# Performance work log

Measured on AMD Instinct MI355X. Metric: run time of the kernel, lower is better.

Reference implementation:

```python
import jax, jax.numpy as jnp
import numpy as np

B, S, D, H, E, K = 4, 2048, 768, 3072, 8, 2
LB_SCALE = 0.01
NOISY_STD = 1.0


def setup_inputs() -> dict:
    key = jax.random.key(0)
    ks = jax.random.split(key, 8)
    x = jax.random.normal(ks[0], (B, S, D), jnp.float32)
    # gate_linear: nn.Linear(D, E, bias=False); torch weight is [E, D]
    gate_w = jax.random.normal(ks[1], (E, D), jnp.float32) * 0.02
    noise_weight = jnp.zeros((E,), jnp.float32)  # initialized to zeros in torch
    noise = jax.random.normal(ks[2], (B, S, E), jnp.float32)  # torch.randn_like(logits)
    # expert weights stored in (in, out) layout: y = x @ w + b
    w1 = jax.random.normal(ks[3], (E, D, H), jnp.float32) * 0.02
    b1 = jnp.zeros((E, H), jnp.float32)
    w2 = jax.random.normal(ks[4], (E, D, H), jnp.float32) * 0.02
    b2 = jnp.zeros((E, H), jnp.float32)
    wp = jax.random.normal(ks[5], (E, H, D), jnp.float32) * 0.02
    bp = jnp.zeros((E, D), jnp.float32)
    return {"x": x, "gate_w": gate_w, "noise_weight": noise_weight, "noise": noise,
            "w1": w1, "b1": b1, "w2": w2, "b2": b2, "wp": wp, "bp": bp}


def reference(x, gate_w, noise_weight, noise, w1, b1, w2, b2, wp, bp):
    num_experts = gate_w.shape[0]
    # --- TopKGateParallel ---
    logits = jnp.einsum('bsd,ed->bse', x, gate_w)            # [B,S,E]
    gate_weights = jax.nn.softmax(logits, axis=-1)
    gate_weights_mean = gate_weights.reshape(-1, num_experts).mean(0)
    uniform = 1.0 / num_experts
    load_balance_loss = jnp.mean((gate_weights_mean - uniform) ** 2) * LB_SCALE
    logits_noisy = logits + noise * NOISY_STD * noise_weight  # noise_weight zeros => no-op at init
    top_k_vals, top_k_ids = jax.lax.top_k(logits_noisy, K)    # [B,S,K]
    # scatter top-k back into a -inf tensor, then softmax -> sparse gates
    topk_mask = jax.nn.one_hot(top_k_ids, num_experts, dtype=logits.dtype).sum(-2) > 0  # [B,S,E]
    sparse_logits = jnp.where(topk_mask, logits_noisy, -jnp.inf)
    gates = jax.nn.softmax(sparse_logits, axis=-1)            # zeros outside top-k
    # --- per-expert SwiGLU, weighted combine (gates are exactly 0 off top-k) ---
    y = jnp.zeros_like(x)
    for e in range(num_experts):  # small fixed expert count
        h = (x @ w1[e] + b1[e]) * jax.nn.silu(x @ w2[e] + b2[e])  # [B,S,H]
        y = y + gates[..., e:e + 1] * (h @ wp[e] + bp[e])
    return y, load_balance_loss
```

## Files before the change

kernel.cpp:

```cpp
#include <hip/hip_runtime.h>
#include <hip/hip_bf16.h>

#define NTOK 8192
#define DDIM 768
#define HDIM 3072
#define NEXP 8
#define MROWS (NTOK*2)
#define RBMAX 32

typedef float f32x4 __attribute__((ext_vector_type(4)));
typedef short bf16x8 __attribute__((ext_vector_type(8)));
typedef unsigned short u16x4 __attribute__((ext_vector_type(4)));

__device__ __forceinline__ unsigned short f2bf(float f) {
  union { float f; unsigned u; } v; v.f = f;
  unsigned r = v.u + 0x7fffu + ((v.u >> 16) & 1u);
  return (unsigned short)(r >> 16);
}

typedef __attribute__((address_space(3))) unsigned int* lds_ptr_t;
typedef const __attribute__((address_space(1))) unsigned int* gbl_ptr_t;
__device__ __forceinline__ void async16(const void* g, void* l) {
  __builtin_amdgcn_global_load_lds((gbl_ptr_t)g, (lds_ptr_t)l, 16, 0, 0);
}

__global__ __launch_bounds__(128) void gating_kernel(
    const float* __restrict__ x, const float* __restrict__ gw,
    const float* __restrict__ nw, const float* __restrict__ noise,
    int* counts, float* sums, int* tok_list, float* gate_list,
    int* tok_top, float* gate_top, int* pos_top)
{
  __shared__ float s_gw[NEXP*DDIM];
  __shared__ float s_sums[NEXP];
  __shared__ float s_nw[NEXP];
  int tid = threadIdx.x;
  for (int i = tid; i < NEXP*DDIM/4; i += 128)
    ((f32x4*)s_gw)[i] = ((const f32x4*)gw)[i];
  if (tid < NEXP) { s_sums[tid] = 0.f; s_nw[tid] = nw[tid]; }
  __syncthreads();
  int t = blockIdx.x*128 + tid;
  float acc[NEXP];
  #pragma unroll
  for (int e = 0; e < NEXP; ++e) acc[e] = 0.f;
  const f32x4* xr = (const f32x4*)(x + (size_t)t*DDIM);
  for (int d4 = 0; d4 < DDIM/4; ++d4) {
    f32x4 xv = xr[d4];
    #pragma unroll
    for (int e = 0; e < NEXP; ++e) {
      f32x4 g = *(const f32x4*)&s_gw[e*DDIM + d4*4];
      acc[e] += xv.x*g.x + xv.y*g.y + xv.z*g.z + xv.w*g.w;
    }
  }
  float m = acc[0];
  #pragma unroll
  for (int e = 1; e < NEXP; ++e) m = fmaxf(m, acc[e]);
  float p[NEXP], s = 0.f;
  #pragma unroll
  for (int e = 0; e < NEXP; ++e) { p[e] = __expf(acc[e]-m); s += p[e]; }
  float inv = 1.f/s;
  #pragma unroll
  for (int e = 0; e < NEXP; ++e) atomicAdd(&s_sums[e], p[e]*inv);
  float ln[NEXP];
  #pragma unroll
  for (int e = 0; e < NEXP; ++e) ln[e] = acc[e] + noise[(size_t)t*NEXP+e]*s_nw[e];
  int i0 = 0; float v0 = ln[0];
  #pragma unroll
  for (int e = 1; e < NEXP; ++e) if (ln[e] > v0) { v0 = ln[e]; i0 = e; }
  int i1 = -1; float v1 = 0.f;
  #pragma unroll
  for (int e = 0; e < NEXP; ++e)
    if (e != i0 && (i1 < 0 || ln[e] > v1)) { v1 = ln[e]; i1 = e; }
  float e1 = __expf(v1 - v0);
  float g0 = 1.f/(1.f + e1);
  float g1 = e1*g0;
  int p0 = atomicAdd(&counts[i0], 1);
  tok_list[i0*NTOK + p0] = t; gate_list[i0*NTOK + p0] = g0;
  int p1 = atomicAdd(&counts[i1], 1);
  tok_list[i1*NTOK + p1] = t; gate_list[i1*NTOK + p1] = g1;
  tok_top[2*t] = i0; tok_top[2*t+1] = i1;
  gate_top[2*t] = g0; gate_top[2*t+1] = g1;
  pos_top[2*t] = p0; pos_top[2*t+1] = p1;
  __syncthreads();
  if (tid < NEXP) atomicAdd(&sums[tid], s_sums[tid]);
}

__global__ void finalize_kernel(const int* counts, const float* sums,
                                int* offsets, float* loss_out)
{
  if (threadIdx.x == 0) {
    int o = 0;
    #pragma unroll
    for (int e = 0; e < NEXP; ++e) { offsets[e] = o; o += counts[e]; }
    offsets[NEXP] = o;
    float l = 0.f;
    #pragma unroll
    for (int e = 0; e < NEXP; ++e) {
      float dv = sums[e]*(1.f/(float)NTOK) - 1.f/(float)NEXP;
      l += dv*dv;
    }
    loss_out[0] = l*(0.01f/(float)NEXP);
  }
}

__global__ __launch_bounds__(256) void cvt_x_kernel(const float* __restrict__ x,
                                                    unsigned short* __restrict__ xb)
{
  int i = blockIdx.x*256 + threadIdx.x;
  f32x4 v = ((const f32x4*)x)[i];
  u16x4 o; o.x = f2bf(v.x); o.y = f2bf(v.y); o.z = f2bf(v.z); o.w = f2bf(v.w);
  ((u16x4*)xb)[i] = o;
}

__global__ __launch_bounds__(256) void transpose_cvt2_kernel(
    const float* __restrict__ src1, unsigned short* __restrict__ dst1,
    const float* __restrict__ src2, unsigned short* __restrict__ dst2,
    int R, int C)
{
  __shared__ unsigned short s[64*65];
  int z = blockIdx.z;
  int e = z & (NEXP-1);
  const float* src = (z < NEXP) ? src1 : src2;
  unsigned short* dst = (z < NEXP) ? dst1 : dst2;
  int r0 = blockIdx.y*64, c0 = blockIdx.x*64;
  const float* sp = src + ((size_t)e*R + r0)*C + c0;
  unsigned short* dp = dst + ((size_t)e*C + c0)*R + r0;
  int t = threadIdx.x;
  #pragma unroll
  for (int i = 0; i < 16; ++i) {
    int idx = t + 256*i;
    int r = idx >> 6, c = idx & 63;
    s[c*65 + r] = f2bf(sp[(size_t)r*C + c]);
  }
  __syncthreads();
  #pragma unroll
  for (int i = 0; i < 16; ++i) {
    int idx = t + 256*i;
    int c = idx >> 6, r = idx & 63;
    dp[(size_t)c*R + r] = s[c*65 + r];
  }
}

__global__ __launch_bounds__(256) void transpose_cvt_kernel(
    const float* __restrict__ src, unsigned short* __restrict__ dst, int R, int C)
{
  __shared__ unsigned short s[64*65];
  int e = blockIdx.z;
  int r0 = blockIdx.y*64, c0 = blockIdx.x*64;
  const float* sp = src + ((size_t)e*R + r0)*C + c0;
  unsigned short* dp = dst + ((size_t)e*C + c0)*R + r0;
  int t = threadIdx.x;
  #pragma unroll
  for (int i = 0; i < 16; ++i) {
    int idx = t + 256*i;
    int r = idx >> 6, c = idx & 63;
    s[c*65 + r] = f2bf(sp[(size_t)r*C + c]);
  }
  __syncthreads();
  #pragma unroll
  for (int i = 0; i < 16; ++i) {
    int idx = t + 256*i;
    int c = idx >> 6, r = idx & 63;
    dp[(size_t)c*R + r] = s[c*65 + r];
  }
}

__global__ __launch_bounds__(256) void compact_kernel(
    const int* __restrict__ counts, const int* __restrict__ offsets,
    const int* __restrict__ tok_list, const float* __restrict__ gate_list,
    int* __restrict__ row_token, float* __restrict__ row_gate)
{
  int e = blockIdx.y;
  int pos = blockIdx.x*256 + threadIdx.x;
  if (pos < counts[e]) {
    int r = offsets[e] + pos;
    row_token[r] = tok_list[e*NTOK + pos];
    row_gate[r]  = gate_list[e*NTOK + pos];
  }
}

__global__ __launch_bounds__(256) void init_y_kernel(
    const int* __restrict__ tok_top, const float* __restrict__ gate_top,
    const float* __restrict__ bp, float* __restrict__ y)
{
  int i = blockIdx.x*256 + threadIdx.x;
  int t = i / (DDIM/4);
  int d4 = i % (DDIM/4);
  int e0 = tok_top[2*t], e1 = tok_top[2*t+1];
  float g0 = gate_top[2*t], g1 = gate_top[2*t+1];
  f32x4 b0 = ((const f32x4*)(bp + (size_t)e0*DDIM))[d4];
  f32x4 b1v = ((const f32x4*)(bp + (size_t)e1*DDIM))[d4];
  ((f32x4*)y)[i] = g0*b0 + g1*b1v;
}

__global__ __launch_bounds__(256) void ffn1_mfma(
    const unsigned short* __restrict__ xb,
    const unsigned short* __restrict__ w1T, const unsigned short* __restrict__ w2T,
    const float* __restrict__ b1, const float* __restrict__ b2,
    const int* __restrict__ offsets, const int* __restrict__ row_token,
    unsigned short* __restrict__ h_buf, int h_base, int HC)
{
  int id = blockIdx.x;
  int e = id & 7;
  int s = id >> 3;
  int rb0 = s & (RBMAX-1);
  int cg = s >> 5;
  int r_lo = offsets[e];
  int rows_e = offsets[e+1] - r_lo;
  int h0 = h_base + cg*64;

  __shared__ __align__(16) char sA[8192];
  __shared__ __align__(16) char sB[8192];
  __shared__ int s_tok[128];

  int tid = threadIdx.x;
  int lane = tid & 63, w = tid >> 6;
  int l16 = lane & 15, quad = lane >> 4;
  int lr = lane >> 2, ls = lane & 3;
  int kseg = ls ^ (lr & 3);
  int fro = l16*64 + ((quad ^ (l16 & 3)) << 4);

  int colB = h0 + w*16 + lr;
  const unsigned short* gB1 = w1T + ((size_t)e*HDIM + colB)*DDIM + kseg*8;
  const unsigned short* gB2 = w2T + ((size_t)e*HDIM + colB)*DDIM + kseg*8;
  char* lA0 = sA + w*1024;
  char* lA1 = sA + (w+4)*1024;
  char* lB1 = sB + w*1024;
  char* lB2 = sB + (w+4)*1024;

  int hcol = h0 + w*16 + l16;
  float bb1 = b1[(size_t)e*HDIM + hcol];
  float bb2 = b2[(size_t)e*HDIM + hcol];
  int hl = hcol - h_base;

  for (int rb = rb0; rb*128 < rows_e; rb += RBMAX) {
    int r0 = r_lo + rb*128;
    int rows_valid = rows_e - rb*128; if (rows_valid > 128) rows_valid = 128;
    __syncthreads();
    if (tid < 128) {
      int r = r0 + tid; if (r > MROWS-1) r = MROWS-1;
      s_tok[tid] = row_token[r];
    }
    __syncthreads();
    const unsigned short* gA0 = xb + (size_t)s_tok[w*16 + lr]*DDIM + kseg*8;
    const unsigned short* gA1 = xb + (size_t)s_tok[(w+4)*16 + lr]*DDIM + kseg*8;

    f32x4 acc1[8], acc2[8];
    #pragma unroll
    for (int i = 0; i < 8; ++i) { acc1[i] = (f32x4){0,0,0,0}; acc2[i] = (f32x4){0,0,0,0}; }

    for (int k0 = 0; k0 < DDIM; k0 += 32) {
      async16(gA0 + k0, lA0);
      async16(gA1 + k0, lA1);
      async16(gB1 + k0, lB1);
      async16(gB2 + k0, lB2);
      __syncthreads();
      bf16x8 bf1 = *(const bf16x8*)(sB + w*1024 + fro);
      bf16x8 bf2 = *(const bf16x8*)(sB + (w+4)*1024 + fro);
      #pragma unroll
      for (int mt = 0; mt < 8; ++mt) {
        bf16x8 af = *(const bf16x8*)(sA + mt*1024 + fro);
        acc1[mt] = __builtin_amdgcn_mfma_f32_16x16x32_bf16(af, bf1, acc1[mt], 0, 0, 0);
        acc2[mt] = __builtin_amdgcn_mfma_f32_16x16x32_bf16(af, bf2, acc2[mt], 0, 0, 0);
      }
      __syncthreads();
    }
    #pragma unroll
    for (int mt = 0; mt < 8; ++mt) {
      #pragma unroll
      for (int r = 0; r < 4; ++r) {
        int row = mt*16 + quad*4 + r;
        if (row < rows_valid) {
          float c1 = acc1[mt][r] + bb1;
          float c2 = acc2[mt][r] + bb2;
          float hv = c1 * (c2 / (1.f + __expf(-c2)));
          h_buf[(size_t)(r0 + row)*HC + hl] = f2bf(hv);
        }
      }
    }
  }
}

__global__ __launch_bounds__(256) void ffn2_mfma(
    const unsigned short* __restrict__ h_buf, const unsigned short* __restrict__ wpT,
    const int* __restrict__ offsets, const int* __restrict__ row_token,
    const float* __restrict__ row_gate, float* __restrict__ outp,
    int h_base, int HC, int mode)
{
  int id = blockIdx.x;
  int e = id & 7;
  int s = id >> 3;
  int rb0 = s & (RBMAX-1);
  int cb = s >> 5;
  int r_lo = offsets[e];
  int rows_e = offsets[e+1] - r_lo;
  int c0 = cb*128;

  __shared__ __align__(16) char sA[8192];
  __shared__ __align__(16) char sB[8192];
  __shared__ int s_tok[128];
  __shared__ float s_gate[128];

  int tid = threadIdx.x;
  int lane = tid & 63, w = tid >> 6;
  int l16 = lane & 15, quad = lane >> 4;
  int lr = lane >> 2, ls = lane & 3;
  int kseg = ls ^ (lr & 3);
  int fro = l16*64 + ((quad ^ (l16 & 3)) << 4);
  int wr = w & 1, wcg = w >> 1;

  const unsigned short* gB0 = wpT + ((size_t)e*DDIM + c0 + w*16 + lr)*HDIM + h_base + kseg*8;
  const unsigned short* gB1 = wpT + ((size_t)e*DDIM + c0 + (w+4)*16 + lr)*HDIM + h_base + kseg*8;
  char* lA0 = sA + w*1024;
  char* lA1 = sA + (w+4)*1024;
  char* lB0 = sB + w*1024;
  char* lB1 = sB + (w+4)*1024;

  for (int rb = rb0; rb*128 < rows_e; rb += RBMAX) {
    int r0 = r_lo + rb*128;
    int rows_valid = rows_e - rb*128; if (rows_valid > 128) rows_valid = 128;
    __syncthreads();
    if (tid < 128) {
      int r = r0 + tid; if (r > MROWS-1) r = MROWS-1;
      s_tok[tid]  = row_token[r];
      s_gate[tid] = row_gate[r];
    }
    __syncthreads();
    int rA0 = r0 + w*16 + lr;     if (rA0 > MROWS-1) rA0 = MROWS-1;
    int rA1 = r0 + (w+4)*16 + lr; if (rA1 > MROWS-1) rA1 = MROWS-1;
    const unsigned short* gA0 = h_buf + (size_t)rA0*HC + kseg*8;
    const unsigned short* gA1 = h_buf + (size_t)rA1*HC + kseg*8;

    f32x4 acc[4][4];
    #pragma unroll
    for (int i = 0; i < 4; ++i)
      #pragma unroll
      for (int j = 0; j < 4; ++j) acc[i][j] = (f32x4){0,0,0,0};

    for (int k0 = 0; k0 < HC; k0 += 32) {
      async16(gA0 + k0, lA0);
      async16(gA1 + k0, lA1);
      async16(gB0 + k0, lB0);
      async16(gB1 + k0, lB1);
      __syncthreads();
      bf16x8 bfr[4];
      #pragma unroll
      for (int nt = 0; nt < 4; ++nt)
        bfr[nt] = *(const bf16x8*)(sB + (wcg*4 + nt)*1024 + fro);
      #pragma unroll
      for (int mt = 0; mt < 4; ++mt) {
        bf16x8 af = *(const bf16x8*)(sA + (wr*4 + mt)*1024 + fro);
        #pragma unroll
        for (int nt = 0; nt < 4; ++nt)
          acc[mt][nt] = __builtin_amdgcn_mfma_f32_16x16x32_bf16(af, bfr[nt], acc[mt][nt], 0, 0, 0);
      }
      __syncthreads();
    }

    if (mode == 0) {
      #pragma unroll
      for (int nt = 0; nt < 4; ++nt) {
        int col = c0 + wcg*64 + nt*16 + l16;
        #pragma unroll
        for (int mt = 0; mt < 4; ++mt) {
          #pragma unroll
          for (int r = 0; r < 4; ++r) {
            int row = wr*64 + mt*16 + quad*4 + r;
            if (row < rows_valid)
              outp[(size_t)(r0 + row)*DDIM + col] = acc[mt][nt][r];
          }
        }
      }
    } else {
      #pragma unroll
      for (int nt = 0; nt < 4; ++nt) {
        int col = c0 + wcg*64 + nt*16 + l16;
        #pragma unroll
        for (int mt = 0; mt < 4; ++mt) {
          #pragma unroll
          for (int r = 0; r < 4; ++r) {
            int row = wr*64 + mt*16 + quad*4 + r;
            if (row < rows_valid)
              atomicAdd(&outp[(size_t)s_tok[row]*DDIM + col], s_gate[row]*acc[mt][nt][r]);
          }
        }
      }
    }
  }
}

__global__ __launch_bounds__(256) void combine_kernel(
    const float* __restrict__ part, const int* __restrict__ tok_top,
    const float* __restrict__ gate_top, const int* __restrict__ pos_top,
    const int* __restrict__ offsets, const float* __restrict__ bp,
    float* __restrict__ y)
{
  int i = blockIdx.x*256 + threadIdx.x;
  int t = i / (DDIM/4);
  int d4 = i % (DDIM/4);
  int e0 = tok_top[2*t], e1 = tok_top[2*t+1];
  float g0 = gate_top[2*t], g1 = gate_top[2*t+1];
  int r0 = offsets[e0] + pos_top[2*t];
  int r1 = offsets[e1] + pos_top[2*t+1];
  f32x4 v0 = ((const f32x4*)part)[(size_t)r0*(DDIM/4) + d4];
  f32x4 v1 = ((const f32x4*)part)[(size_t)r1*(DDIM/4) + d4];
  f32x4 b0 = ((const f32x4*)(bp + (size_t)e0*DDIM))[d4];
  f32x4 b1v = ((const f32x4*)(bp + (size_t)e1*DDIM))[d4];
  ((f32x4*)y)[i] = g0*(v0 + b0) + g1*(v1 + b1v);
}

__global__ __launch_bounds__(256) void ffn2_kernel(
    const unsigned short* __restrict__ h_buf, const float* __restrict__ wp,
    const int* __restrict__ offsets, const int* __restrict__ row_token,
    const float* __restrict__ row_gate, float* __restrict__ y, int h_base, int HC)
{
  int e = blockIdx.z;
  int r_lo = offsets[e];
  int rows_e = offsets[e+1] - r_lo;
  int bx = blockIdx.x;
  if (bx*128 >= rows_e) return;
  int r0 = r_lo + bx*128;
  int rows_valid = rows_e - bx*128; if (rows_valid > 128) rows_valid = 128;
  int c0 = blockIdx.y*128;

  __shared__ unsigned short sA[128*40];
  __shared__ int s_tok[128];
  __shared__ float s_gate[128];

  int tid = threadIdx.x;
  if (tid < 128) {
    int r = r0 + tid; if (r > MROWS-1) r = MROWS-1;
    s_tok[tid]  = row_token[r];
    s_gate[tid] = row_gate[r];
  }
  int lane = tid & 63;
  int wc = tid >> 6;
  int quad = lane >> 4, l16 = lane & 15;

  const float* wp0 = wp + (size_t)e*HDIM*DDIM + c0 + wc*32 + l16;

  f32x4 acc[8][2];
  #pragma unroll
  for (int i = 0; i < 8; ++i) { acc[i][0] = (f32x4){0,0,0,0}; acc[i][1] = (f32x4){0,0,0,0}; }
  __syncthreads();

  for (int k0 = 0; k0 < HC; k0 += 32) {
    #pragma unroll
    for (int i = 0; i < 2; ++i) {
      int c = i*256 + tid;
      int row = c >> 2, k8 = c & 3;
      int rr = r0 + row; if (rr > MROWS-1) rr = MROWS-1;
      bf16x8 v = *(const bf16x8*)(h_buf + (size_t)rr*HC + k0 + k8*8);
      *(bf16x8*)&sA[row*40 + k8*8] = v;
    }
    float bv[2][8];
    #pragma unroll
    for (int nt = 0; nt < 2; ++nt)
      #pragma unroll
      for (int j = 0; j < 8; ++j)
        bv[nt][j] = wp0[(size_t)(h_base + k0 + quad*8 + j)*DDIM + nt*16];
    bf16x8 bfr[2];
    #pragma unroll
    for (int nt = 0; nt < 2; ++nt)
      #pragma unroll
      for (int j = 0; j < 8; ++j) bfr[nt][j] = (short)f2bf(bv[nt][j]);
    __syncthreads();
    #pragma unroll
    for (int mt = 0; mt < 8; ++mt) {
      bf16x8 af = *(const bf16x8*)&sA[(mt*16 + l16)*40 + quad*8];
      acc[mt][0] = __builtin_amdgcn_mfma_f32_16x16x32_bf16(af, bfr[0], acc[mt][0], 0, 0, 0);
      acc[mt][1] = __builtin_amdgcn_mfma_f32_16x16x32_bf16(af, bfr[1], acc[mt][1], 0, 0, 0);
    }
    __syncthreads();
  }
  #pragma unroll
  for (int nt = 0; nt < 2; ++nt) {
    int col = c0 + wc*32 + nt*16 + l16;
    #pragma unroll
    for (int mt = 0; mt < 8; ++mt) {
      #pragma unroll
      for (int r = 0; r < 4; ++r) {
        int row = mt*16 + quad*4 + r;
        if (row < rows_valid)
          atomicAdd(&y[(size_t)s_tok[row]*DDIM + col], s_gate[row]*acc[mt][nt][r]);
      }
    }
  }
}

extern "C" void kernel_launch(void* const* d_in, const int* in_sizes, int n_in,
                              void* d_out, int out_size, void* d_ws, size_t ws_size,
                              hipStream_t stream)
{
  (void)in_sizes; (void)n_in; (void)out_size;
  const float* x     = (const float*)d_in[0];
  const float* gw    = (const float*)d_in[1];
  const float* nw    = (const float*)d_in[2];
  const float* noise = (const float*)d_in[3];
  const float* w1    = (const float*)d_in[4];
  const float* b1    = (const float*)d_in[5];
  const float* w2    = (const float*)d_in[6];
  const float* b2    = (const float*)d_in[7];
  const float* wp    = (const float*)d_in[8];
  const float* bp    = (const float*)d_in[9];
  float* y = (float*)d_out;

  char* ws = (char*)d_ws;
  int*   counts   = (int*)(ws + 0);
  float* sums     = (float*)(ws + 64);
  int*   offsets  = (int*)(ws + 128);
  size_t off = 256;
  int*   tok_list  = (int*)(ws + off);   off += (size_t)NEXP*NTOK*4;
  float* gate_list = (float*)(ws + off); off += (size_t)NEXP*NTOK*4;
  int*   tok_top   = (int*)(ws + off);   off += (size_t)NTOK*2*4;
  float* gate_top  = (float*)(ws + off); off += (size_t)NTOK*2*4;
  int*   pos_top   = (int*)(ws + off);   off += (size_t)NTOK*2*4;
  int*   row_token = (int*)(ws + off);   off += (size_t)MROWS*4;
  float* row_gate  = (float*)(ws + off); off += (size_t)MROWS*4;
  unsigned short* xb = (unsigned short*)(ws + off); off += (size_t)NTOK*DDIM*2;

  const size_t WT    = (size_t)NEXP*DDIM*HDIM*2;
  const size_t HFULL = (size_t)MROWS*HDIM*2;
  const size_t PSZ   = (size_t)MROWS*DDIM*4;

  unsigned short* w1T = (unsigned short*)(ws + off);
  unsigned short* w2T = (unsigned short*)(ws + off + WT);
  unsigned short* wpT = (unsigned short*)(ws + off + 2*WT);

  bool tierA = (off + 3*WT + HFULL + PSZ <= ws_size);
  bool haveP = (off + 3*WT + (size_t)MROWS*128*2 <= ws_size);
  size_t oH = off + (haveP ? 3*WT : 2*WT);

  int HC;
  unsigned short* h_buf;
  float* part = nullptr;
  if (tierA) {
    HC = HDIM;
    h_buf = (unsigned short*)(ws + off + 3*WT);
    part  = (float*)(ws + off + 3*WT + HFULL);
  } else {
    static const int hc_opts[6] = {3072, 1536, 768, 384, 192, 128};
    HC = 128;
    for (int i = 0; i < 6; ++i)
      if (oH + (size_t)MROWS*hc_opts[i]*2 <= ws_size) { HC = hc_opts[i]; break; }
    h_buf = (unsigned short*)(ws + oH);
  }

  hipMemsetAsync(d_ws, 0, 256, stream);
  cvt_x_kernel<<<NTOK*DDIM/1024, 256, 0, stream>>>(x, xb);
  transpose_cvt2_kernel<<<dim3(HDIM/64, DDIM/64, NEXP*2), 256, 0, stream>>>(
      w1, w1T, w2, w2T, DDIM, HDIM);
  if (haveP)
    transpose_cvt_kernel<<<dim3(DDIM/64, HDIM/64, NEXP), 256, 0, stream>>>(wp, wpT, HDIM, DDIM);

  gating_kernel<<<NTOK/128, 128, 0, stream>>>(x, gw, nw, noise, counts, sums,
                                              tok_list, gate_list, tok_top, gate_top, pos_top);
  finalize_kernel<<<1, 64, 0, stream>>>(counts, sums, offsets, y + (size_t)NTOK*DDIM);
  compact_kernel<<<dim3(NTOK/256, NEXP), 256, 0, stream>>>(counts, offsets, tok_list,
                                                           gate_list, row_token, row_gate);

  if (tierA) {
    ffn1_mfma<<<NEXP*(HDIM/64)*RBMAX, 256, 0, stream>>>(xb, w1T, w2T, b1, b2, offsets,
                                                        row_token, h_buf, 0, HC);
    ffn2_mfma<<<NEXP*(DDIM/128)*RBMAX, 256, 0, stream>>>(h_buf, wpT, offsets, row_token,
                                                         row_gate, part, 0, HC, 0);
    combine_kernel<<<NTOK*DDIM/1024, 256, 0, stream>>>(part, tok_top, gate_top, pos_top,
                                                       offsets, bp, y);
  } else {
    init_y_kernel<<<NTOK*DDIM/1024, 256, 0, stream>>>(tok_top, gate_top, bp, y);
    int nch = HDIM / HC;
    for (int c = 0; c < nch; ++c) {
      ffn1_mfma<<<NEXP*(HC/64)*RBMAX, 256, 0, stream>>>(xb, w1T, w2T, b1, b2, offsets,
                                                        row_token, h_buf, c*HC, HC);
      if (haveP)
        ffn2_mfma<<<NEXP*(DDIM/128)*RBMAX, 256, 0, stream>>>(h_buf, wpT, offsets, row_token,
                                                             row_gate, y, c*HC, HC, 1);
      else
        ffn2_kernel<<<dim3(128, DDIM/128, NEXP), 256, 0, stream>>>(h_buf, wp, offsets, row_token,
                                                                   row_gate, y, c*HC, HC);
    }
  }
}
```

Baseline: 823.8 us.

## Double-buffer LDS in expert GEMMs and fuse x bf16 conversion into gating

The two expert GEMM kernels now use double-buffered shared memory. The async global-to-LDS loads for the next K-step are issued before the MFMAs on the current buffer, and one of the two barriers per iteration is dropped. The gating kernel is restructured to use one wavefront per token with a shuffle reduction. It also writes the bf16 copy of x, which removes the separate conversion kernel and a second read of x. The cost is twice the LDS per block, which may lower occupancy, and the gating kernel now issues many more, smaller blocks.

```diff
diff --git a/kernel.cpp b/kernel.cpp
--- a/kernel.cpp
+++ b/kernel.cpp
@@ -24,9 +24,10 @@
   __builtin_amdgcn_global_load_lds((gbl_ptr_t)g, (lds_ptr_t)l, 16, 0, 0);
 }
 
-__global__ __launch_bounds__(128) void gating_kernel(
+__global__ __launch_bounds__(256) void gating_kernel(
     const float* __restrict__ x, const float* __restrict__ gw,
     const float* __restrict__ nw, const float* __restrict__ noise,
+    unsigned short* __restrict__ xb,
     int* counts, float* sums, int* tok_list, float* gate_list,
     int* tok_top, float* gate_top, int* pos_top)
 {
@@ -34,22 +35,35 @@
   __shared__ float s_sums[NEXP];
   __shared__ float s_nw[NEXP];
   int tid = threadIdx.x;
-  for (int i = tid; i < NEXP*DDIM/4; i += 128)
+  for (int i = tid; i < NEXP*DDIM/4; i += 256)
     ((f32x4*)s_gw)[i] = ((const f32x4*)gw)[i];
   if (tid < NEXP) { s_sums[tid] = 0.f; s_nw[tid] = nw[tid]; }
   __syncthreads();
-  int t = blockIdx.x*128 + tid;
+  int wv = tid >> 6, lane = tid & 63;
+  int t = blockIdx.x*4 + wv;
+
   float acc[NEXP];
   #pragma unroll
   for (int e = 0; e < NEXP; ++e) acc[e] = 0.f;
-  const f32x4* xr = (const f32x4*)(x + (size_t)t*DDIM);
-  for (int d4 = 0; d4 < DDIM/4; ++d4) {
-    f32x4 xv = xr[d4];
+  const f32x4* xr = (const f32x4*)x + (size_t)t*(DDIM/4);
+  u16x4* xbw = (u16x4*)xb + (size_t)t*(DDIM/4);
+  #pragma unroll
+  for (int j = 0; j < 3; ++j) {
+    f32x4 xv = xr[j*64 + lane];
+    u16x4 o; o.x = f2bf(xv.x); o.y = f2bf(xv.y); o.z = f2bf(xv.z); o.w = f2bf(xv.w);
+    xbw[j*64 + lane] = o;
     #pragma unroll
     for (int e = 0; e < NEXP; ++e) {
-      f32x4 g = *(const f32x4*)&s_gw[e*DDIM + d4*4];
+      f32x4 g = ((const f32x4*)s_gw)[e*(DDIM/4) + j*64 + lane];
       acc[e] += xv.x*g.x + xv.y*g.y + xv.z*g.z + xv.w*g.w;
     }
+  }
+  #pragma unroll
+  for (int e = 0; e < NEXP; ++e) {
+    float v = acc[e];
+    #pragma unroll
+    for (int off = 32; off >= 1; off >>= 1) v += __shfl_xor(v, off, 64);
+    acc[e] = v;
   }
   float m = acc[0];
   #pragma unroll
@@ -58,8 +72,6 @@
   #pragma unroll
   for (int e = 0; e < NEXP; ++e) { p[e] = __expf(acc[e]-m); s += p[e]; }
   float inv = 1.f/s;
-  #pragma unroll
-  for (int e = 0; e < NEXP; ++e) atomicAdd(&s_sums[e], p[e]*inv);
   float ln[NEXP];
   #pragma unroll
   for (int e = 0; e < NEXP; ++e) ln[e] = acc[e] + noise[(size_t)t*NEXP+e]*s_nw[e];
@@ -73,13 +85,17 @@
   float e1 = __expf(v1 - v0);
   float g0 = 1.f/(1.f + e1);
   float g1 = e1*g0;
-  int p0 = atomicAdd(&counts[i0], 1);
-  tok_list[i0*NTOK + p0] = t; gate_list[i0*NTOK + p0] = g0;
-  int p1 = atomicAdd(&counts[i1], 1);
-  tok_list[i1*NTOK + p1] = t; gate_list[i1*NTOK + p1] = g1;
-  tok_top[2*t] = i0; tok_top[2*t+1] = i1;
-  gate_top[2*t] = g0; gate_top[2*t+1] = g1;
-  pos_top[2*t] = p0; pos_top[2*t+1] = p1;
+  if (lane == 0) {
+    #pragma unroll
+    for (int e = 0; e < NEXP; ++e) atomicAdd(&s_sums[e], p[e]*inv);
+    int p0 = atomicAdd(&counts[i0], 1);
+    tok_list[i0*NTOK + p0] = t; gate_list[i0*NTOK + p0] = g0;
+    int p1 = atomicAdd(&counts[i1], 1);
+    tok_list[i1*NTOK + p1] = t; gate_list[i1*NTOK + p1] = g1;
+    tok_top[2*t] = i0; tok_top[2*t+1] = i1;
+    gate_top[2*t] = g0; gate_top[2*t+1] = g1;
+    pos_top[2*t] = p0; pos_top[2*t+1] = p1;
+  }
   __syncthreads();
   if (tid < NEXP) atomicAdd(&sums[tid], s_sums[tid]);
 }
@@ -100,15 +116,6 @@
     }
     loss_out[0] = l*(0.01f/(float)NEXP);
   }
-}
-
-__global__ __launch_bounds__(256) void cvt_x_kernel(const float* __restrict__ x,
-                                                    unsigned short* __restrict__ xb)
-{
-  int i = blockIdx.x*256 + threadIdx.x;
-  f32x4 v = ((const f32x4*)x)[i];
-  u16x4 o; o.x = f2bf(v.x); o.y = f2bf(v.y); o.z = f2bf(v.z); o.w = f2bf(v.w);
-  ((u16x4*)xb)[i] = o;
 }
 
 __global__ __launch_bounds__(256) void transpose_cvt2_kernel(
@@ -208,8 +215,8 @@
   int rows_e = offsets[e+1] - r_lo;
   int h0 = h_base + cg*64;
 
-  __shared__ __align__(16) char sA[8192];
-  __shared__ __align__(16) char sB[8192];
+  __shared__ __align__(16) char sA[2][8192];
+  __shared__ __align__(16) char sB[2][8192];
   __shared__ int s_tok[128];
 
   int tid = threadIdx.x;
@@ -222,10 +229,6 @@
   int colB = h0 + w*16 + lr;
   const unsigned short* gB1 = w1T + ((size_t)e*HDIM + colB)*DDIM + kseg*8;
   const unsigned short* gB2 = w2T + ((size_t)e*HDIM + colB)*DDIM + kseg*8;
-  char* lA0 = sA + w*1024;
-  char* lA1 = sA + (w+4)*1024;
-  char* lB1 = sB + w*1024;
-  char* lB2 = sB + (w+4)*1024;
 
   int hcol = h0 + w*16 + l16;
   float bb1 = b1[(size_t)e*HDIM + hcol];
@@ -244,25 +247,42 @@
     const unsigned short* gA0 = xb + (size_t)s_tok[w*16 + lr]*DDIM + kseg*8;
     const unsigned short* gA1 = xb + (size_t)s_tok[(w+4)*16 + lr]*DDIM + kseg*8;
 
+    async16(gA0, sA[0] + w*1024);
+    async16(gA1, sA[0] + (w+4)*1024);
+    async16(gB1, sB[0] + w*1024);
+    async16(gB2, sB[0] + (w+4)*1024);
+
     f32x4 acc1[8], acc2[8];
     #pragma unroll
     for (int i = 0; i < 8; ++i) { acc1[i] = (f32x4){0,0,0,0}; acc2[i] = (f32x4){0,0,0,0}; }
 
-    for (int k0 = 0; k0 < DDIM; k0 += 32) {
-      async16(gA0 + k0, lA0);
-      async16(gA1 + k0, lA1);
-      async16(gB1 + k0, lB1);
-      async16(gB2 + k0, lB2);
+    int p = 0;
+    for (int k0 = 0; k0 < DDIM-32; k0 += 32) {
       __syncthreads();
-      bf16x8 bf1 = *(const bf16x8*)(sB + w*1024 + fro);
-      bf16x8 bf2 = *(const bf16x8*)(sB + (w+4)*1024 + fro);
+      async16(gA0 + k0+32, sA[p^1] + w*1024);
+      async16(gA1 + k0+32, sA[p^1] + (w+4)*1024);
+      async16(gB1 + k0+32, sB[p^1] + w*1024);
+      async16(gB2 + k0+32, sB[p^1] + (w+4)*1024);
+      bf16x8 bf1 = *(const bf16x8*)(sB[p] + w*1024 + fro);
+      bf16x8 bf2 = *(const bf16x8*)(sB[p] + (w+4)*1024 + fro);
       #pragma unroll
       for (int mt = 0; mt < 8; ++mt) {
-        bf16x8 af = *(const bf16x8*)(sA + mt*1024 + fro);
+        bf16x8 af = *(const bf16x8*)(sA[p] + mt*1024 + fro);
         acc1[mt] = __builtin_amdgcn_mfma_f32_16x16x32_bf16(af, bf1, acc1[mt], 0, 0, 0);
         acc2[mt] = __builtin_amdgcn_mfma_f32_16x16x32_bf16(af, bf2, acc2[mt], 0, 0, 0);
       }
-      __syncthreads();
+      p ^= 1;
+    }
+    __syncthreads();
+    {
+      bf16x8 bf1 = *(const bf16x8*)(sB[p] + w*1024 + fro);
+      bf16x8 bf2 = *(const bf16x8*)(sB[p] + (w+4)*1024 + fro);
+      #pragma unroll
+      for (int mt = 0; mt < 8; ++mt) {
+        bf16x8 af = *(const bf16x8*)(sA[p] + mt*1024 + fro);
+        acc1[mt] = __builtin_amdgcn_mfma_f32_16x16x32_bf16(af, bf1, acc1[mt], 0, 0, 0);
+        acc2[mt] = __builtin_amdgcn_mfma_f32_16x16x32_bf16(af, bf2, acc2[mt], 0, 0, 0);
+      }
     }
     #pragma unroll
     for (int mt = 0; mt < 8; ++mt) {
@@ -295,8 +315,8 @@
   int rows_e = offsets[e+1] - r_lo;
   int c0 = cb*128;
 
-  __shared__ __align__(16) char sA[8192];
-  __shared__ __align__(16) char sB[8192];
+  __shared__ __align__(16) char sA[2][8192];
+  __shared__ __align__(16) char sB[2][8192];
   __shared__ int s_tok[128];
   __shared__ float s_gate[128];
 
@@ -310,10 +330,6 @@
 
   const unsigned short* gB0 = wpT + ((size_t)e*DDIM + c0 + w*16 + lr)*HDIM + h_base + kseg*8;
   const unsigned short* gB1 = wpT + ((size_t)e*DDIM + c0 + (w+4)*16 + lr)*HDIM + h_base + kseg*8;
-  char* lA0 = sA + w*1024;
-  char* lA1 = sA + (w+4)*1024;
-  char* lB0 = sB + w*1024;
-  char* lB1 = sB + (w+4)*1024;
 
   for (int rb = rb0; rb*128 < rows_e; rb += RBMAX) {
     int r0 = r_lo + rb*128;
@@ -330,30 +346,50 @@
     const unsigned short* gA0 = h_buf + (size_t)rA0*HC + kseg*8;
     const unsigned short* gA1 = h_buf + (size_t)rA1*HC + kseg*8;
 
+    async16(gA0, sA[0] + w*1024);
+    async16(gA1, sA[0] + (w+4)*1024);
+    async16(gB0, sB[0] + w*1024);
+    async16(gB1, sB[0] + (w+4)*1024);
+
     f32x4 acc[4][4];
     #pragma unroll
     for (int i = 0; i < 4; ++i)
       #pragma unroll
       for (int j = 0; j < 4; ++j) acc[i][j] = (f32x4){0,0,0,0};
 
-    for (int k0 = 0; k0 < HC; k0 += 32) {
-      async16(gA0 + k0, lA0);
-      async16(gA1 + k0, lA1);
-      async16(gB0 + k0, lB0);
-      async16(gB1 + k0, lB1);
+    int p = 0;
+    for (int k0 = 0; k0 < HC-32; k0 += 32) {
       __syncthreads();
+      async16(gA0 + k0+32, sA[p^1] + w*1024);
+      async16(gA1 + k0+32, sA[p^1] + (w+4)*1024);
+      async16(gB0 + k0+32, sB[p^1] + w*1024);
+      async16(gB1 + k0+32, sB[p^1] + (w+4)*1024);
       bf16x8 bfr[4];
       #pragma unroll
       for (int nt = 0; nt < 4; ++nt)
-        bfr[nt] = *(const bf16x8*)(sB + (wcg*4 + nt)*1024 + fro);
+        bfr[nt] = *(const bf16x8*)(sB[p] + (wcg*4 + nt)*1024 + fro);
       #pragma unroll
       for (int mt = 0; mt < 4; ++mt) {
-        bf16x8 af = *(const bf16x8*)(sA + (wr*4 + mt)*1024 + fro);
+        bf16x8 af = *(const bf16x8*)(sA[p] + (wr*4 + mt)*1024 + fro);
         #pragma unroll
         for (int nt = 0; nt < 4; ++nt)
           acc[mt][nt] = __builtin_amdgcn_mfma_f32_16x16x32_bf16(af, bfr[nt], acc[mt][nt], 0, 0, 0);
       }
-      __syncthreads();
+      p ^= 1;
+    }
+    __syncthreads();
+    {
+      bf16x8 bfr[4];
+      #pragma unroll
+      for (int nt = 0; nt < 4; ++nt)
+        bfr[nt] = *(const bf16x8*)(sB[p] + (wcg*4 + nt)*1024 + fro);
+      #pragma unroll
+      for (int mt = 0; mt < 4; ++mt) {
+        bf16x8 af = *(const bf16x8*)(sA[p] + (wr*4 + mt)*1024 + fro);
+        #pragma unroll
+        for (int nt = 0; nt < 4; ++nt)
+          acc[mt][nt] = __builtin_amdgcn_mfma_f32_16x16x32_bf16(af, bfr[nt], acc[mt][nt], 0, 0, 0);
+      }
     }
 
     if (mode == 0) {
@@ -546,14 +582,13 @@
   }
 
   hipMemsetAsync(d_ws, 0, 256, stream);
-  cvt_x_kernel<<<NTOK*DDIM/1024, 256, 0, stream>>>(x, xb);
   transpose_cvt2_kernel<<<dim3(HDIM/64, DDIM/64, NEXP*2), 256, 0, stream>>>(
       w1, w1T, w2, w2T, DDIM, HDIM);
   if (haveP)
     transpose_cvt_kernel<<<dim3(DDIM/64, HDIM/64, NEXP), 256, 0, stream>>>(wp, wpT, HDIM, DDIM);
 
-  gating_kernel<<<NTOK/128, 128, 0, stream>>>(x, gw, nw, noise, counts, sums,
-                                              tok_list, gate_list, tok_top, gate_top, pos_top);
+  gating_kernel<<<NTOK/4, 256, 0, stream>>>(x, gw, nw, noise, xb, counts, sums,
+                                            tok_list, gate_list, tok_top, gate_top, pos_top);
   finalize_kernel<<<1, 64, 0, stream>>>(counts, sums, offsets, y + (size_t)NTOK*DDIM);
   compact_kernel<<<dim3(NTOK/256, NEXP), 256, 0, stream>>>(counts, offsets, tok_list,
                                                            gate_list, row_token, row_gate);
```

Measured after the change: 1.245 ms. 1.51x slower.
